# Kernel optimization log

Hardware: AMD Instinct MI355X
Metric: run time of the kernel (lower is better)

Reference implementation:

```python
import jax, jax.numpy as jnp
import numpy as np

# Static taxonomy layout (closed over; mirrors __init__ args La/layers)
LAYER_SIZES = (100, 1000, 5000, 13900)
LAYER_STARTS = tuple(int(s) for s in np.cumsum((0,) + LAYER_SIZES)[:-1])
N_NODES = int(sum(LAYER_SIZES))
H = len(LAYER_SIZES)
BATCH = 4096


def setup_inputs() -> dict:
    key = jax.random.key(0)
    y_pred = jax.random.normal(key, (BATCH, N_NODES), dtype=jnp.float32)

    rng = np.random.default_rng(0)
    # parents[v] = global index of v's parent in the previous layer
    parents = np.zeros(N_NODES, np.int32)
    for l in range(1, H):
        s, n = LAYER_STARTS[l], LAYER_SIZES[l]
        ps, pn = LAYER_STARTS[l - 1], LAYER_SIZES[l - 1]
        parents[s:s + n] = rng.integers(ps, ps + pn, size=n)

    # hierarchy-consistent one-hot targets: pick a leaf, mark it and all ancestors
    leaf = rng.integers(LAYER_STARTS[H - 1], N_NODES, size=BATCH)
    y_true = np.zeros((BATCH, N_NODES), np.float32)
    node = leaf
    rows = np.arange(BATCH)
    for l in range(H - 1, 0, -1):
        y_true[rows, node] = 1.0
        node = parents[node]
    y_true[rows, node] = 1.0  # layer-0 ancestor

    alpha_layer = jnp.array([0.0, 1.0, 1.0, 1.0], dtype=jnp.float32)
    return {
        "y_pred": y_pred,
        "y_true": jnp.asarray(y_true),
        "parents": jnp.asarray(parents),
        "alpha_layer": alpha_layer,
    }


def reference(y_pred, y_true, parents, alpha_layer):
    # Fused, batched version of the per-sample / per-layer Python loops.
    loss = jnp.float32(0.0)
    for l in range(1, H):  # small static loop over taxonomy layers
        s, n = LAYER_STARTS[l], LAYER_SIZES[l]
        ps, pn = LAYER_STARTS[l - 1], LAYER_SIZES[l - 1]

        logits = y_pred[:, s:s + n]                      # [B, n_l]
        p = jax.nn.softmax(logits, axis=1)               # outer softmax (as in source)
        # nn.CrossEntropyLoss with probability targets == -sum(t * log_softmax(input));
        # the source feeds the already-softmaxed p (double softmax) -> reproduce exactly.
        cce = -jnp.sum(y_true[:, s:s + n] * jax.nn.log_softmax(p, axis=1), axis=1)  # [B]

        # hierarchical dependency: child prob must not exceed its parent's prob
        pp = jax.nn.softmax(y_pred[:, ps:ps + pn], axis=1)   # [B, n_{l-1}]
        pidx = parents[s:s + n] - ps                         # local parent ids [n_l]
        d = jnp.mean(jax.nn.relu(p - pp[:, pidx]), axis=1)   # [B]

        loss = loss + jnp.mean(cce + d) * alpha_layer[l]
    return loss
```

## Files before the change

kernel.cpp:

```cpp
#include <hip/hip_runtime.h>
#include <math.h>

#define BATCH   4096
#define N_NODES 20000
#define H       4
#define BLOCK   512
#define NW      (BLOCK / 64)

constexpr int LSTART_C[H] = {0, 100, 1100, 6100};
constexpr int LSIZE_C[H]  = {100, 1000, 5000, 13900};
constexpr float LOGS_C[H] = {0.f, 6.9087547793f, 8.5173931714f, 9.5397160591f};

__device__ __forceinline__ float waveSum(float v) {
#pragma unroll
    for (int off = 32; off > 0; off >>= 1) v += __shfl_xor(v, off);
    return v;
}
__device__ __forceinline__ float bf2f(ushort h) {
    return __uint_as_float(((unsigned)h) << 16);
}
__device__ __forceinline__ ushort f2bf_trunc(float x) {
    return (ushort)(__float_as_uint(x) >> 16);
}

template<int L>
__device__ __forceinline__ void p1_layer(const float4* __restrict__ yp4,
                                         const float4* __restrict__ yt4,
                                         ushort* row_bf,
                                         float& z, float& dt, const int tid)
{
    constexpr int SQ = LSTART_C[L] / 4, NQ = LSIZE_C[L] / 4;

    auto body = [&](int i, const float4& v, const float4& t) {
        float e0 = __expf(v.x), e1 = __expf(v.y), e2 = __expf(v.z), e3 = __expf(v.w);
        ushort4 h;
        h.x = f2bf_trunc(e0); h.y = f2bf_trunc(e1);
        h.z = f2bf_trunc(e2); h.w = f2bf_trunc(e3);
        *reinterpret_cast<ushort4*>(&row_bf[4 * (SQ + i)]) = h;
        z += (e0 + e1) + (e2 + e3);
        if constexpr (L > 0) {
            dt += t.x * e0 + t.y * e1 + t.z * e2 + t.w * e3;
        }
    };

    int i = tid;
    for (; i + BLOCK < NQ; i += 2 * BLOCK) {
        float4 va = yp4[SQ + i];
        float4 vb = yp4[SQ + i + BLOCK];
        float4 ta{}, tb{};
        if constexpr (L > 0) { ta = yt4[SQ + i]; tb = yt4[SQ + i + BLOCK]; }
        body(i, va, ta);
        body(i + BLOCK, vb, tb);
    }
    if (i < NQ) {
        float4 v = yp4[SQ + i];
        float4 t{};
        if constexpr (L > 0) t = yt4[SQ + i];
        body(i, v, t);
    }
}

template<int L>
__device__ __forceinline__ void p2_layer(const int4* __restrict__ pa4,
                                         const ushort* row_bf,
                                         const float invZ, const float invZp,
                                         float& D, const int tid)
{
    constexpr int S = LSTART_C[L], SQ = S / 4, NQ = LSIZE_C[L] / 4;

    auto body = [&](const int4& pa, const ushort4& h) {
        float p0 = bf2f(h.x) * invZ, p1 = bf2f(h.y) * invZ;
        float p2 = bf2f(h.z) * invZ, p3 = bf2f(h.w) * invZ;
        float pp0 = bf2f(row_bf[pa.x]) * invZp, pp1 = bf2f(row_bf[pa.y]) * invZp;
        float pp2 = bf2f(row_bf[pa.z]) * invZp, pp3 = bf2f(row_bf[pa.w]) * invZp;
        D += (fmaxf(p0 - pp0, 0.f) + fmaxf(p1 - pp1, 0.f))
           + (fmaxf(p2 - pp2, 0.f) + fmaxf(p3 - pp3, 0.f));
    };

    int i = tid;
    for (; i + BLOCK < NQ; i += 2 * BLOCK) {
        int4 paa = pa4[SQ + i];
        int4 pab = pa4[SQ + i + BLOCK];
        ushort4 ha = *reinterpret_cast<const ushort4*>(&row_bf[S + 4 * i]);
        ushort4 hb = *reinterpret_cast<const ushort4*>(&row_bf[S + 4 * (i + BLOCK)]);
        body(paa, ha);
        body(pab, hb);
    }
    if (i < NQ) {
        int4 pa = pa4[SQ + i];
        ushort4 h = *reinterpret_cast<const ushort4*>(&row_bf[S + 4 * i]);
        body(pa, h);
    }
}

__global__ __launch_bounds__(BLOCK, 8) void tax_main(
    const float* __restrict__ y_pred,
    const float* __restrict__ y_true,
    const int*   __restrict__ parents,
    const float* __restrict__ alpha,
    float*       __restrict__ partial)
{
    __shared__ __align__(8) ushort row_bf[N_NODES];
    __shared__ float sc[NW * 12];

    const int tid = threadIdx.x;
    const int b   = blockIdx.x;
    const int wid = tid >> 6;
    const int lid = tid & 63;

    const float4* yp4 = reinterpret_cast<const float4*>(y_pred + (size_t)b * N_NODES);
    const float4* yt4 = reinterpret_cast<const float4*>(y_true + (size_t)b * N_NODES);
    const int4*   pa4 = reinterpret_cast<const int4*>(parents);

    {
        float z = 0.f, dt = 0.f;
        p1_layer<0>(yp4, yt4, row_bf, z, dt, tid);
        z = waveSum(z);
        if (lid == 0) sc[wid * 12 + 0] = z;
    }
    {
        float z = 0.f, dt = 0.f;
        p1_layer<1>(yp4, yt4, row_bf, z, dt, tid);
        z = waveSum(z); dt = waveSum(dt);
        if (lid == 0) { sc[wid * 12 + 1] = z; sc[wid * 12 + 2] = dt; }
    }
    {
        float z = 0.f, dt = 0.f;
        p1_layer<2>(yp4, yt4, row_bf, z, dt, tid);
        z = waveSum(z); dt = waveSum(dt);
        if (lid == 0) { sc[wid * 12 + 3] = z; sc[wid * 12 + 4] = dt; }
    }
    {
        float z = 0.f, dt = 0.f;
        p1_layer<3>(yp4, yt4, row_bf, z, dt, tid);
        z = waveSum(z); dt = waveSum(dt);
        if (lid == 0) { sc[wid * 12 + 5] = z; sc[wid * 12 + 6] = dt; }
    }
    __syncthreads();

    float z0 = 0.f, z1 = 0.f, z2 = 0.f, z3 = 0.f;
#pragma unroll
    for (int w = 0; w < NW; ++w) {
        const float* p = &sc[w * 12];
        z0 += p[0]; z1 += p[1]; z2 += p[3]; z3 += p[5];
    }
    const float iZ0 = __builtin_amdgcn_rcpf(z0);
    const float iZ1 = __builtin_amdgcn_rcpf(z1);
    const float iZ2 = __builtin_amdgcn_rcpf(z2);
    const float iZ3 = __builtin_amdgcn_rcpf(z3);

    float D1 = 0.f, D2 = 0.f, D3 = 0.f;
    p2_layer<1>(pa4, row_bf, iZ1, iZ0, D1, tid);
    p2_layer<2>(pa4, row_bf, iZ2, iZ1, D2, tid);
    p2_layer<3>(pa4, row_bf, iZ3, iZ2, D3, tid);
    D1 = waveSum(D1); D2 = waveSum(D2); D3 = waveSum(D3);
    if (lid == 0) { sc[wid * 12 + 8] = D1; sc[wid * 12 + 9] = D2; sc[wid * 12 + 10] = D3; }
    __syncthreads();

    if (tid == 0) {
        float dt1 = 0.f, dt2 = 0.f, dt3 = 0.f;
        float Dl1 = 0.f, Dl2 = 0.f, Dl3 = 0.f;
        for (int w = 0; w < NW; ++w) {
            const float* p = &sc[w * 12];
            dt1 += p[2]; dt2 += p[4]; dt3 += p[6];
            Dl1 += p[8]; Dl2 += p[9]; Dl3 += p[10];
        }
        float loss = alpha[1] * (LOGS_C[1] - dt1 * iZ1 + Dl1 / (float)LSIZE_C[1])
                   + alpha[2] * (LOGS_C[2] - dt2 * iZ2 + Dl2 / (float)LSIZE_C[2])
                   + alpha[3] * (LOGS_C[3] - dt3 * iZ3 + Dl3 / (float)LSIZE_C[3]);
        partial[b] = loss;
    }
}

__global__ __launch_bounds__(1024) void tax_reduce(
    const float* __restrict__ partial, float* __restrict__ out)
{
    __shared__ float red[16];
    const int tid = threadIdx.x, wid = tid >> 6, lid = tid & 63;
    float v = 0.f;
    for (int i = tid; i < BATCH; i += 1024) v += partial[i];
    v = waveSum(v);
    if (lid == 0) red[wid] = v;
    __syncthreads();
    if (wid == 0) {
        float x = (lid < 16) ? red[lid] : 0.f;
        x = waveSum(x);
        if (lid == 0) out[0] = x * (1.0f / (float)BATCH);
    }
}

extern "C" void kernel_launch(void* const* d_in, const int* in_sizes, int n_in,
                              void* d_out, int out_size, void* d_ws, size_t ws_size,
                              hipStream_t stream) {
    const float* y_pred  = (const float*)d_in[0];
    const float* y_true  = (const float*)d_in[1];
    const int*   parents = (const int*)d_in[2];
    const float* alpha   = (const float*)d_in[3];
    float* partial = (float*)d_ws;
    float* out     = (float*)d_out;

    tax_main<<<dim3(BATCH), dim3(BLOCK), 0, stream>>>(y_pred, y_true, parents, alpha, partial);
    tax_reduce<<<dim3(1), dim3(1024), 0, stream>>>(partial, out);
}
```

Baseline: 123.4 us.

## Stop staging leaf layer in LDS; recompute leaf exp from global in pass two

Only layers 0-2 are now staged in LDS as bf16, which shrinks shared memory per block from about 40KB to about 12KB. The leaf-layer dependency term re-reads y_pred from global, likely hitting L2, and recomputes exp instead of reading staged values. Block size drops from 512 to 256 threads. Smaller LDS allows more resident blocks per CU, at the cost of a second global read and a second exp over the largest layer.

```diff
diff --git a/kernel.cpp b/kernel.cpp
--- a/kernel.cpp
+++ b/kernel.cpp
@@ -3,8 +3,9 @@
 
 #define BATCH   4096
 #define N_NODES 20000
+#define N_LDS   6100
 #define H       4
-#define BLOCK   512
+#define BLOCK   256
 #define NW      (BLOCK / 64)
 
 constexpr int LSTART_C[H] = {0, 100, 1100, 6100};
@@ -23,7 +24,7 @@
     return (ushort)(__float_as_uint(x) >> 16);
 }
 
-template<int L>
+template<int L, bool STAGE>
 __device__ __forceinline__ void p1_layer(const float4* __restrict__ yp4,
                                          const float4* __restrict__ yt4,
                                          ushort* row_bf,
@@ -33,10 +34,12 @@
 
     auto body = [&](int i, const float4& v, const float4& t) {
         float e0 = __expf(v.x), e1 = __expf(v.y), e2 = __expf(v.z), e3 = __expf(v.w);
-        ushort4 h;
-        h.x = f2bf_trunc(e0); h.y = f2bf_trunc(e1);
-        h.z = f2bf_trunc(e2); h.w = f2bf_trunc(e3);
-        *reinterpret_cast<ushort4*>(&row_bf[4 * (SQ + i)]) = h;
+        if constexpr (STAGE) {
+            ushort4 h;
+            h.x = f2bf_trunc(e0); h.y = f2bf_trunc(e1);
+            h.z = f2bf_trunc(e2); h.w = f2bf_trunc(e3);
+            *reinterpret_cast<ushort4*>(&row_bf[4 * (SQ + i)]) = h;
+        }
         z += (e0 + e1) + (e2 + e3);
         if constexpr (L > 0) {
             dt += t.x * e0 + t.y * e1 + t.z * e2 + t.w * e3;
@@ -93,6 +96,35 @@
     }
 }
 
+__device__ __forceinline__ void d3_layer(const float4* __restrict__ yp4,
+                                         const int4* __restrict__ pa4,
+                                         const ushort* row_bf,
+                                         const float invZ, const float invZp,
+                                         float& D, const int tid)
+{
+    constexpr int SQ = LSTART_C[3] / 4, NQ = LSIZE_C[3] / 4;
+
+    auto body = [&](const float4& v, const int4& pa) {
+        float p0 = __expf(v.x) * invZ, p1 = __expf(v.y) * invZ;
+        float p2 = __expf(v.z) * invZ, p3 = __expf(v.w) * invZ;
+        float pp0 = bf2f(row_bf[pa.x]) * invZp, pp1 = bf2f(row_bf[pa.y]) * invZp;
+        float pp2 = bf2f(row_bf[pa.z]) * invZp, pp3 = bf2f(row_bf[pa.w]) * invZp;
+        D += (fmaxf(p0 - pp0, 0.f) + fmaxf(p1 - pp1, 0.f))
+           + (fmaxf(p2 - pp2, 0.f) + fmaxf(p3 - pp3, 0.f));
+    };
+
+    int i = tid;
+    for (; i + BLOCK < NQ; i += 2 * BLOCK) {
+        float4 va = yp4[SQ + i];
+        float4 vb = yp4[SQ + i + BLOCK];
+        int4 paa = pa4[SQ + i];
+        int4 pab = pa4[SQ + i + BLOCK];
+        body(va, paa);
+        body(vb, pab);
+    }
+    if (i < NQ) body(yp4[SQ + i], pa4[SQ + i]);
+}
+
 __global__ __launch_bounds__(BLOCK, 8) void tax_main(
     const float* __restrict__ y_pred,
     const float* __restrict__ y_true,
@@ -100,7 +132,7 @@
     const float* __restrict__ alpha,
     float*       __restrict__ partial)
 {
-    __shared__ __align__(8) ushort row_bf[N_NODES];
+    __shared__ __align__(8) ushort row_bf[N_LDS];
     __shared__ float sc[NW * 12];
 
     const int tid = threadIdx.x;
@@ -114,25 +146,25 @@
 
     {
         float z = 0.f, dt = 0.f;
-        p1_layer<0>(yp4, yt4, row_bf, z, dt, tid);
+        p1_layer<0, true>(yp4, yt4, row_bf, z, dt, tid);
         z = waveSum(z);
         if (lid == 0) sc[wid * 12 + 0] = z;
     }
     {
         float z = 0.f, dt = 0.f;
-        p1_layer<1>(yp4, yt4, row_bf, z, dt, tid);
+        p1_layer<1, true>(yp4, yt4, row_bf, z, dt, tid);
         z = waveSum(z); dt = waveSum(dt);
         if (lid == 0) { sc[wid * 12 + 1] = z; sc[wid * 12 + 2] = dt; }
     }
     {
         float z = 0.f, dt = 0.f;
-        p1_layer<2>(yp4, yt4, row_bf, z, dt, tid);
+        p1_layer<2, true>(yp4, yt4, row_bf, z, dt, tid);
         z = waveSum(z); dt = waveSum(dt);
         if (lid == 0) { sc[wid * 12 + 3] = z; sc[wid * 12 + 4] = dt; }
     }
     {
         float z = 0.f, dt = 0.f;
-        p1_layer<3>(yp4, yt4, row_bf, z, dt, tid);
+        p1_layer<3, false>(yp4, yt4, row_bf, z, dt, tid);
         z = waveSum(z); dt = waveSum(dt);
         if (lid == 0) { sc[wid * 12 + 5] = z; sc[wid * 12 + 6] = dt; }
     }
@@ -150,9 +182,9 @@
     const float iZ3 = __builtin_amdgcn_rcpf(z3);
 
     float D1 = 0.f, D2 = 0.f, D3 = 0.f;
+    d3_layer(yp4, pa4, row_bf, iZ3, iZ2, D3, tid);
     p2_layer<1>(pa4, row_bf, iZ1, iZ0, D1, tid);
     p2_layer<2>(pa4, row_bf, iZ2, iZ1, D2, tid);
-    p2_layer<3>(pa4, row_bf, iZ3, iZ2, D3, tid);
     D1 = waveSum(D1); D2 = waveSum(D2); D3 = waveSum(D3);
     if (lid == 0) { sc[wid * 12 + 8] = D1; sc[wid * 12 + 9] = D2; sc[wid * 12 + 10] = D3; }
     __syncthreads();
```

Result: slower. 138.1 us (+11.9%).
